# Performance work log

Measured on AMD Instinct MI355X. Metric: run time of the kernel, lower is better.

Reference implementation:

```python
import jax, jax.numpy as jnp
import numpy as np

N_USER = 50000
N_ITEM = 100000
N = N_USER + N_ITEM
NNZ = 3_000_000
EMB = 64
BATCH = 4096


def _l2norm(x, eps=1e-12):
    # torch F.normalize(p=2, dim=1): x / max(||x||, eps)
    n = jnp.sqrt(jnp.sum(x * x, axis=1, keepdims=True))
    return x / jnp.maximum(n, eps)


def setup_inputs() -> dict:
    key = jax.random.key(0)
    ks = jax.random.split(key, 12)
    users = jax.random.randint(ks[0], (BATCH,), 0, N_USER, dtype=jnp.int64 if jax.config.jax_enable_x64 else jnp.int32)
    rows = jax.random.randint(ks[1], (NNZ,), 0, N, dtype=jnp.int32)
    cols = jax.random.randint(ks[2], (NNZ,), 0, N, dtype=jnp.int32)
    vals = jax.random.uniform(ks[3], (NNZ,), dtype=jnp.float32)
    user_emb = jax.random.normal(ks[4], (N_USER, EMB), dtype=jnp.float32) * 0.1
    item_emb = jax.random.normal(ks[5], (N_ITEM, EMB), dtype=jnp.float32) * 0.1
    W0 = jax.random.normal(ks[6], (EMB, EMB), dtype=jnp.float32) * 0.1
    b0 = jax.random.normal(ks[7], (1, EMB), dtype=jnp.float32) * 0.1
    W1 = jax.random.normal(ks[8], (EMB, EMB), dtype=jnp.float32) * 0.1
    b1 = jax.random.normal(ks[9], (1, EMB), dtype=jnp.float32) * 0.1
    W2 = jax.random.normal(ks[10], (EMB, EMB), dtype=jnp.float32) * 0.1
    b2 = jax.random.normal(ks[11], (1, EMB), dtype=jnp.float32) * 0.1
    return {"users": users, "rows": rows, "cols": cols, "vals": vals,
            "user_emb": user_emb, "item_emb": item_emb,
            "W0": W0, "b0": b0, "W1": W1, "b1": b1, "W2": W2, "b2": b2}


def reference(users, rows, cols, vals, user_emb, item_emb, W0, b0, W1, b1, W2, b2):
    ego = jnp.concatenate([user_emb, item_emb], axis=0)  # [N, EMB]
    total = ego  # all_embeddings[0]
    for W, b in ((W0, b0), (W1, b1), (W2, b2)):
        # SpMM: side[r] = sum_e vals[e] * ego[cols[e]] for rows[e]==r
        side = jax.ops.segment_sum(vals[:, None] * ego[cols], rows, num_segments=N)
        ego = jax.nn.leaky_relu(side @ W + b, negative_slope=0.2)
        total = total + _l2norm(ego)
    u_g = total[:N_USER]
    return u_g[users]  # [BATCH, EMB]
```

## Files before the change

### kernel.cpp

```cpp
#include <hip/hip_runtime.h>
#include <hip/hip_fp16.h>

#define N_USER 50000
#define N_ITEM 100000
#define NTOT   150000
#define NNZ    3000000
#define EMB    64
#define BATCH  4096

#define BROWS  128
#define NB     1172
#define BCAP   3008
#define CHUNK  6144
#define WIN    12288
#define SSTR   67

#define SCALE  262144.0f
#define INVSC  (1.0f / 262144.0f)

typedef unsigned short u16;
typedef unsigned int   u32;
typedef _Float16 f16;
typedef f16   f16x8 __attribute__((ext_vector_type(8)));
typedef float f32x4 __attribute__((ext_vector_type(4)));

__global__ __launch_bounds__(256) void k_init_ego(const float4* __restrict__ ue,
                                                  const float4* __restrict__ ie,
                                                  uint2* __restrict__ ego) {
    int i = blockIdx.x * 256 + threadIdx.x;
    const int UF4 = N_USER * EMB / 4;
    float4 f = (i < UF4) ? ue[i] : ie[i - UF4];
    __half2 h0 = __floats2half2_rn(f.x, f.y);
    __half2 h1 = __floats2half2_rn(f.z, f.w);
    ego[i] = make_uint2(*(u32*)&h0, *(u32*)&h1);
}

__global__ __launch_bounds__(256) void k_init_out(const float* __restrict__ ue,
                                                  const int* __restrict__ users,
                                                  float* __restrict__ out) {
    int t = blockIdx.x * 256 + threadIdx.x;
    int w = t >> 6, lane = t & 63;
    int u = users[w];
    out[w * EMB + lane] = ue[(size_t)u * EMB + lane];
}

__device__ __forceinline__ void scan_excl(const int* src, int* dst, int* ws8,
                                          int tid, int lane, int w) {
    int carry = 0;
    for (int base = 0; base < NB; base += 512) {
        int i = base + tid;
        int x = (i < NB) ? src[i] : 0;
        int v = x;
#pragma unroll
        for (int off = 1; off < 64; off <<= 1) {
            int y = __shfl_up(v, off);
            if (lane >= off) v += y;
        }
        if (lane == 63) ws8[w] = v;
        __syncthreads();
        if (tid < 8) {
            int s = ws8[tid];
#pragma unroll
            for (int off = 1; off < 8; off <<= 1) {
                int y = __shfl_up(s, off);
                if (tid >= off) s += y;
            }
            ws8[tid] = s;
        }
        __syncthreads();
        int excl = carry + (w ? ws8[w - 1] : 0) + v - x;
        if (i < NB) dst[i] = excl;
        carry += ws8[7];
        __syncthreads();
    }
}

__global__ __launch_bounds__(512) void k_bucket(const int* __restrict__ rows,
                                                const int* __restrict__ cols,
                                                const float* __restrict__ vals,
                                                int* __restrict__ bcnt,
                                                int2* __restrict__ bbuf) {
    __shared__ int2 stage[CHUNK];
    __shared__ u16  sbuck[CHUNK];
    __shared__ int histA[NB], histB[NB], cur[NB], gbase[NB];
    __shared__ int ws8[8];
    int tid = threadIdx.x, lane = tid & 63, w = tid >> 6;
    int start = blockIdx.x * WIN;
    int s2    = start + CHUNK;
    int n1 = min(start + CHUNK, NNZ) - start; n1 = n1 < 0 ? 0 : n1;
    int n2 = min(s2 + CHUNK, NNZ) - s2;       n2 = n2 < 0 ? 0 : n2;

    for (int i = tid; i < NB; i += 512) { histA[i] = 0; histB[i] = 0; }
    __syncthreads();
    for (int i = tid; i < n1; i += 512)
        atomicAdd(&histA[rows[start + i] >> 7], 1);
    for (int i = tid; i < n2; i += 512)
        atomicAdd(&histB[rows[s2 + i] >> 7], 1);
    __syncthreads();

    for (int i = tid; i < NB; i += 512) {
        int t = histA[i] + histB[i];
        gbase[i] = t ? atomicAdd(&bcnt[i * 16], t) : 0;
    }
    scan_excl(histA, cur, ws8, tid, lane, w);

    for (int i = tid; i < n1; i += 512) {
        int e = start + i;
        int r = rows[e];
        int b = r >> 7;
        int pos = atomicAdd(&cur[b], 1);
        stage[pos] = make_int2(cols[e] | ((r & 127) << 18), __float_as_int(vals[e]));
        sbuck[pos] = (u16)b;
    }
    __syncthreads();
    for (int j = tid; j < n1; j += 512) {
        int b = sbuck[j];
        int pos = gbase[b] + (j - (cur[b] - histA[b]));
        if (pos < BCAP)
            bbuf[(size_t)b * BCAP + pos] = stage[j];
    }
    __syncthreads();

    scan_excl(histB, cur, ws8, tid, lane, w);
    for (int i = tid; i < n2; i += 512) {
        int e = s2 + i;
        int r = rows[e];
        int b = r >> 7;
        int pos = atomicAdd(&cur[b], 1);
        stage[pos] = make_int2(cols[e] | ((r & 127) << 18), __float_as_int(vals[e]));
        sbuck[pos] = (u16)b;
    }
    __syncthreads();
    for (int j = tid; j < n2; j += 512) {
        int b = sbuck[j];
        int pos = gbase[b] + histA[b] + (j - (cur[b] - histB[b]));
        if (pos < BCAP)
            bbuf[(size_t)b * BCAP + pos] = stage[j];
    }
}

__global__ __launch_bounds__(512) void k_fused(const int* __restrict__ bcnt,
                                               const int2* __restrict__ bbuf,
                                               const f16* __restrict__ ego_in,
                                               const float* __restrict__ W,
                                               const float* __restrict__ bias,
                                               u16* __restrict__ ego_out) {
    __shared__ int S[BROWS * SSTR];
    __shared__ f16 Wl[64 * 72];
    int tid = threadIdx.x;
    for (int i = tid; i < BROWS * SSTR; i += 512) S[i] = 0;
    for (int i = tid; i < 4096; i += 512) {
        int k = i >> 6, n = i & 63;
        Wl[n * 72 + k] = (f16)W[i];
    }
    __syncthreads();

    int b = blockIdx.x;
    int cnt = min(bcnt[b * 16], BCAP);
    const int2* src = bbuf + (size_t)b * BCAP;
    int slot = tid >> 3;
    int d8   = tid & 7;
    const char* egob = (const char*)ego_in;

    for (int it0 = 0; it0 < cnt; it0 += 512) {
        int2  pr[8];
        float mk[8];
        uint4 g[8];
#pragma unroll
        for (int u = 0; u < 8; ++u) {
            int ee = it0 + slot + u * 64;
            int ec = min(ee, cnt - 1);
            pr[u] = src[ec];
            mk[u] = (ee < cnt) ? SCALE : 0.f;
        }
#pragma unroll
        for (int u = 0; u < 8; ++u) {
            int col = pr[u].x & 0x3FFFF;
            g[u] = *(const uint4*)(egob + ((size_t)col << 7) + d8 * 16);
        }
#pragma unroll
        for (int u = 0; u < 8; ++u) {
            float vs = __int_as_float(pr[u].y) * mk[u];
            int rl = ((u32)pr[u].x) >> 18;
            float2 f0 = __half22float2(*(const __half2*)&g[u].x);
            float2 f1 = __half22float2(*(const __half2*)&g[u].y);
            float2 f2 = __half22float2(*(const __half2*)&g[u].z);
            float2 f3 = __half22float2(*(const __half2*)&g[u].w);
            int* sp = &S[rl * SSTR + d8 * 4];
            atomicAdd(sp + 0,  (int)(vs * f0.x));
            atomicAdd(sp + 32, (int)(vs * f0.y));
            atomicAdd(sp + 1,  (int)(vs * f1.x));
            atomicAdd(sp + 33, (int)(vs * f1.y));
            atomicAdd(sp + 2,  (int)(vs * f2.x));
            atomicAdd(sp + 34, (int)(vs * f2.y));
            atomicAdd(sp + 3,  (int)(vs * f3.x));
            atomicAdd(sp + 35, (int)(vs * f3.y));
        }
    }
    __syncthreads();

    int lane = tid & 63, w = tid >> 6;
    int m = lane & 15, quad = lane >> 4;
    int rowbase = b * BROWS;
    int m0 = w * 16;
    f32x4 C[4] = {{0.f,0.f,0.f,0.f},{0.f,0.f,0.f,0.f},{0.f,0.f,0.f,0.f},{0.f,0.f,0.f,0.f}};
#pragma unroll
    for (int kk = 0; kk < 2; ++kk) {
        const int* ap = &S[(m0 + m) * SSTR + kk * 16 + quad * 4];
        f16x8 A;
#pragma unroll
        for (int c = 0; c < 4; ++c) {
            A[2 * c]     = (f16)((float)ap[c]      * INVSC);
            A[2 * c + 1] = (f16)((float)ap[c + 32] * INVSC);
        }
#pragma unroll
        for (int nt = 0; nt < 4; ++nt) {
            f16x8 B = *(const f16x8*)&Wl[(nt * 16 + m) * 72 + kk * 32 + quad * 8];
            C[nt] = __builtin_amdgcn_mfma_f32_16x16x32_f16(A, B, C[nt], 0, 0, 0);
        }
    }
#pragma unroll
    for (int nt = 0; nt < 4; ++nt) {
        float bv = bias[nt * 16 + m];
#pragma unroll
        for (int r = 0; r < 4; ++r) {
            int orow = rowbase + m0 + quad * 4 + r;
            float o = C[nt][r] + bv;
            o = o > 0.f ? o : 0.2f * o;
            if (orow < NTOT) {
                __half hh = __float2half(o);
                ego_out[(size_t)orow * EMB + nt * 16 + m] = *(u16*)&hh;
            }
        }
    }
}

__global__ __launch_bounds__(256) void k_accum(const __half* __restrict__ ego,
                                               const int* __restrict__ users,
                                               float* __restrict__ out) {
    int t = blockIdx.x * 256 + threadIdx.x;
    int w = t >> 6, lane = t & 63;
    int u = users[w];
    float x = __half2float(ego[(size_t)u * EMB + lane]);
    float ss = x * x;
#pragma unroll
    for (int off = 32; off; off >>= 1) ss += __shfl_xor(ss, off);
    float n = sqrtf(ss);
    out[w * EMB + lane] += x / fmaxf(n, 1e-12f);
}

extern "C" void kernel_launch(void* const* d_in, const int* in_sizes, int n_in,
                              void* d_out, int out_size, void* d_ws, size_t ws_size,
                              hipStream_t stream) {
    const int*   users = (const int*)d_in[0];
    const int*   rows  = (const int*)d_in[1];
    const int*   cols  = (const int*)d_in[2];
    const float* vals  = (const float*)d_in[3];
    const float* ue    = (const float*)d_in[4];
    const float* ie    = (const float*)d_in[5];
    const float* Ws[3] = {(const float*)d_in[6], (const float*)d_in[8], (const float*)d_in[10]};
    const float* bs[3] = {(const float*)d_in[7], (const float*)d_in[9], (const float*)d_in[11]};
    float* out = (float*)d_out;

    char* p = (char*)d_ws;
    f16*  egoA  = (f16*)p;  p += (size_t)NTOT * EMB * 2;
    f16*  egoB  = (f16*)p;  p += (size_t)NTOT * EMB * 2;
    int2* bbuf  = (int2*)p; p += (size_t)NB * BCAP * 8;
    int*  bcnt  = (int*)p;  p += (size_t)NB * 16 * 4;

    hipMemsetAsync(bcnt, 0, (size_t)NB * 16 * 4, stream);
    k_init_ego<<<NTOT * EMB / 4 / 256, 256, 0, stream>>>(
        (const float4*)ue, (const float4*)ie, (uint2*)egoA);
    k_init_out<<<(BATCH * EMB) / 256, 256, 0, stream>>>(ue, users, out);

    k_bucket<<<(NNZ + WIN - 1) / WIN, 512, 0, stream>>>(rows, cols, vals, bcnt, bbuf);

    const int grids[3] = {NB, NB, (N_USER + BROWS - 1) / BROWS};
    f16* bufs[2] = {egoA, egoB};
    for (int l = 0; l < 3; ++l) {
        const f16* src = bufs[l & 1];
        f16*       dst = bufs[(l + 1) & 1];
        k_fused<<<grids[l], 512, 0, stream>>>(bcnt, bbuf, src, Ws[l], bs[l], (u16*)dst);
        k_accum<<<(BATCH * EMB) / 256, 256, 0, stream>>>((const __half*)dst, users, out);
    }
}
```

Before: 371.7 us.

## Sort bucket edges by row in LDS and accumulate SpMM in registers

Each block now builds a per-row CSR of its bucket in shared memory (histogram, prefix scan, scatter) and then has 8 lanes per row accumulate the gathered embeddings in fp32 registers. This replaces the fixed-point integer LDS atomics (8 atomics per edge) and the int-to-half conversion before the MFMA. The intent is to remove LDS atomic contention and the quantisation step. In exchange the kernel does two extra passes over the edge list plus more barriers, and skewed per-row degrees can cause wave divergence in the gather loop.

```diff
diff --git a/kernel.cpp b/kernel.cpp
--- a/kernel.cpp
+++ b/kernel.cpp
@@ -13,10 +13,6 @@
 #define BCAP   3008
 #define CHUNK  6144
 #define WIN    12288
-#define SSTR   67
-
-#define SCALE  262144.0f
-#define INVSC  (1.0f / 262144.0f)
 
 typedef unsigned short u16;
 typedef unsigned int   u32;
@@ -145,74 +141,114 @@
                                                const float* __restrict__ W,
                                                const float* __restrict__ bias,
                                                u16* __restrict__ ego_out) {
-    __shared__ int S[BROWS * SSTR];
-    __shared__ f16 Wl[64 * 72];
-    int tid = threadIdx.x;
-    for (int i = tid; i < BROWS * SSTR; i += 512) S[i] = 0;
+    __shared__ int2 stg[BCAP];
+    __shared__ f16  S16[BROWS * 72];
+    __shared__ f16  Wl[64 * 72];
+    __shared__ int  hist[128], cur[128], rowptr[129];
+    __shared__ int  ws2[2];
+    int tid = threadIdx.x, lane = tid & 63, w = tid >> 6;
+
+    int b = blockIdx.x;
+    int cnt = min(bcnt[b * 16], BCAP);
+    const int2* src = bbuf + (size_t)b * BCAP;
+
     for (int i = tid; i < 4096; i += 512) {
         int k = i >> 6, n = i & 63;
         Wl[n * 72 + k] = (f16)W[i];
     }
-    __syncthreads();
-
-    int b = blockIdx.x;
-    int cnt = min(bcnt[b * 16], BCAP);
-    const int2* src = bbuf + (size_t)b * BCAP;
-    int slot = tid >> 3;
-    int d8   = tid & 7;
+    if (tid < 128) hist[tid] = 0;
+    __syncthreads();
+
+    for (int i = tid; i < cnt; i += 512)
+        atomicAdd(&hist[((u32)src[i].x >> 18) & 127], 1);
+    __syncthreads();
+
+    int sx = 0, sv = 0;
+    if (tid < 128) {
+        sx = hist[tid]; sv = sx;
+#pragma unroll
+        for (int off = 1; off < 64; off <<= 1) {
+            int y = __shfl_up(sv, off);
+            if (lane >= off) sv += y;
+        }
+        if (lane == 63) ws2[tid >> 6] = sv;
+    }
+    __syncthreads();
+    if (tid < 128) {
+        int excl = sv - sx + ((tid >= 64) ? ws2[0] : 0);
+        rowptr[tid] = excl;
+        cur[tid]    = excl;
+    }
+    if (tid == 0) rowptr[128] = cnt;
+    __syncthreads();
+
+    for (int i = tid; i < cnt; i += 512) {
+        int2 e = src[i];
+        int pos = atomicAdd(&cur[((u32)e.x >> 18) & 127], 1);
+        stg[pos] = e;
+    }
+    __syncthreads();
+
     const char* egob = (const char*)ego_in;
-
-    for (int it0 = 0; it0 < cnt; it0 += 512) {
-        int2  pr[8];
-        float mk[8];
-        uint4 g[8];
-#pragma unroll
-        for (int u = 0; u < 8; ++u) {
-            int ee = it0 + slot + u * 64;
-            int ec = min(ee, cnt - 1);
-            pr[u] = src[ec];
-            mk[u] = (ee < cnt) ? SCALE : 0.f;
-        }
-#pragma unroll
-        for (int u = 0; u < 8; ++u) {
-            int col = pr[u].x & 0x3FFFF;
-            g[u] = *(const uint4*)(egob + ((size_t)col << 7) + d8 * 16);
-        }
-#pragma unroll
-        for (int u = 0; u < 8; ++u) {
-            float vs = __int_as_float(pr[u].y) * mk[u];
-            int rl = ((u32)pr[u].x) >> 18;
-            float2 f0 = __half22float2(*(const __half2*)&g[u].x);
-            float2 f1 = __half22float2(*(const __half2*)&g[u].y);
-            float2 f2 = __half22float2(*(const __half2*)&g[u].z);
-            float2 f3 = __half22float2(*(const __half2*)&g[u].w);
-            int* sp = &S[rl * SSTR + d8 * 4];
-            atomicAdd(sp + 0,  (int)(vs * f0.x));
-            atomicAdd(sp + 32, (int)(vs * f0.y));
-            atomicAdd(sp + 1,  (int)(vs * f1.x));
-            atomicAdd(sp + 33, (int)(vs * f1.y));
-            atomicAdd(sp + 2,  (int)(vs * f2.x));
-            atomicAdd(sp + 34, (int)(vs * f2.y));
-            atomicAdd(sp + 3,  (int)(vs * f3.x));
-            atomicAdd(sp + 35, (int)(vs * f3.y));
-        }
-    }
-    __syncthreads();
-
-    int lane = tid & 63, w = tid >> 6;
+    int slot = lane >> 3, d8 = lane & 7;
+#pragma unroll
+    for (int rb = 0; rb < 2; ++rb) {
+        int r  = w * 16 + rb * 8 + slot;
+        int e  = rowptr[r];
+        int k1 = rowptr[r + 1];
+        float acc[8];
+#pragma unroll
+        for (int j = 0; j < 8; ++j) acc[j] = 0.f;
+        while (__any(e < k1)) {
+            bool c0 = e < k1, c1 = (e + 1) < k1;
+            uint4 g0, g1;
+            float v0 = 0.f, v1 = 0.f;
+            if (c0) {
+                int2 p = stg[e];
+                g0 = *(const uint4*)(egob + ((size_t)(p.x & 0x3FFFF) << 7) + d8 * 16);
+                v0 = __int_as_float(p.y);
+            }
+            if (c1) {
+                int2 p = stg[e + 1];
+                g1 = *(const uint4*)(egob + ((size_t)(p.x & 0x3FFFF) << 7) + d8 * 16);
+                v1 = __int_as_float(p.y);
+            }
+            if (c0) {
+                float2 f0 = __half22float2(*(const __half2*)&g0.x);
+                float2 f1 = __half22float2(*(const __half2*)&g0.y);
+                float2 f2 = __half22float2(*(const __half2*)&g0.z);
+                float2 f3 = __half22float2(*(const __half2*)&g0.w);
+                acc[0] = fmaf(v0, f0.x, acc[0]); acc[1] = fmaf(v0, f0.y, acc[1]);
+                acc[2] = fmaf(v0, f1.x, acc[2]); acc[3] = fmaf(v0, f1.y, acc[3]);
+                acc[4] = fmaf(v0, f2.x, acc[4]); acc[5] = fmaf(v0, f2.y, acc[5]);
+                acc[6] = fmaf(v0, f3.x, acc[6]); acc[7] = fmaf(v0, f3.y, acc[7]);
+            }
+            if (c1) {
+                float2 f0 = __half22float2(*(const __half2*)&g1.x);
+                float2 f1 = __half22float2(*(const __half2*)&g1.y);
+                float2 f2 = __half22float2(*(const __half2*)&g1.z);
+                float2 f3 = __half22float2(*(const __half2*)&g1.w);
+                acc[0] = fmaf(v1, f0.x, acc[0]); acc[1] = fmaf(v1, f0.y, acc[1]);
+                acc[2] = fmaf(v1, f1.x, acc[2]); acc[3] = fmaf(v1, f1.y, acc[3]);
+                acc[4] = fmaf(v1, f2.x, acc[4]); acc[5] = fmaf(v1, f2.y, acc[5]);
+                acc[6] = fmaf(v1, f3.x, acc[6]); acc[7] = fmaf(v1, f3.y, acc[7]);
+            }
+            e += 2;
+        }
+        f16x8 h;
+#pragma unroll
+        for (int j = 0; j < 8; ++j) h[j] = (f16)acc[j];
+        *(f16x8*)&S16[r * 72 + d8 * 8] = h;
+    }
+    __syncthreads();
+
     int m = lane & 15, quad = lane >> 4;
     int rowbase = b * BROWS;
     int m0 = w * 16;
     f32x4 C[4] = {{0.f,0.f,0.f,0.f},{0.f,0.f,0.f,0.f},{0.f,0.f,0.f,0.f},{0.f,0.f,0.f,0.f}};
 #pragma unroll
     for (int kk = 0; kk < 2; ++kk) {
-        const int* ap = &S[(m0 + m) * SSTR + kk * 16 + quad * 4];
-        f16x8 A;
-#pragma unroll
-        for (int c = 0; c < 4; ++c) {
-            A[2 * c]     = (f16)((float)ap[c]      * INVSC);
-            A[2 * c + 1] = (f16)((float)ap[c + 32] * INVSC);
-        }
+        f16x8 A = *(const f16x8*)&S16[(m0 + m) * 72 + kk * 32 + quad * 8];
 #pragma unroll
         for (int nt = 0; nt < 4; ++nt) {
             f16x8 B = *(const f16x8*)&Wl[(nt * 16 + m) * 72 + kk * 32 + quad * 8];
```

New measurement: 359.7 us. 3.2% less time.
